# Kernel optimization log

Hardware: AMD Instinct MI355X
Metric: run time of the kernel (lower is better)

Reference implementation:

```python
import math
import jax, jax.numpy as jnp
import numpy as np

D_MODEL = 1024
NUM_HEAD = 16
HEAD_DIM = 64
B = 4
S = 1024


def setup_inputs() -> dict:
    key = jax.random.key(0)
    ks = jax.random.split(key, 11)
    scale = 1.0 / math.sqrt(D_MODEL)
    inp = {
        "x": jax.random.normal(ks[0], (B, S, D_MODEL), dtype=jnp.float32),
        "y": jax.random.normal(ks[1], (B, S, D_MODEL), dtype=jnp.float32),
        "mask": jnp.zeros((S, S), dtype=jnp.float32),
        "Wq": jax.random.uniform(ks[2], (D_MODEL, D_MODEL), jnp.float32, -scale, scale),
        "bq": jax.random.uniform(ks[3], (D_MODEL,), jnp.float32, -scale, scale),
        "Wk": jax.random.uniform(ks[4], (D_MODEL, D_MODEL), jnp.float32, -scale, scale),
        "bk": jax.random.uniform(ks[5], (D_MODEL,), jnp.float32, -scale, scale),
        "Wv": jax.random.uniform(ks[6], (D_MODEL, D_MODEL), jnp.float32, -scale, scale),
        "bv": jax.random.uniform(ks[7], (D_MODEL,), jnp.float32, -scale, scale),
        "Wo": jax.random.uniform(ks[8], (D_MODEL, D_MODEL), jnp.float32, -scale, scale),
        "bo": jax.random.uniform(ks[9], (D_MODEL,), jnp.float32, -scale, scale),
    }
    return inp


def _split_heads(t):
    # (B, S, D) -> (B, H, S, hd)
    b, s, _ = t.shape
    return t.reshape(b, s, NUM_HEAD, HEAD_DIM).transpose(0, 2, 1, 3)


def reference(x, y, mask, Wq, bq, Wk, bk, Wv, bv, Wo, bo):
    q = _split_heads(y @ Wq.T + bq)  # (B, H, S, hd)
    k = _split_heads(x @ Wk.T + bk)
    v = _split_heads(x @ Wv.T + bv)
    scaled = jnp.einsum("bhqd,bhkd->bhqk", q, k) / math.sqrt(HEAD_DIM)
    # torch: scaled.permute(1,0,2,3) + mask  -> (H, B, S, S); second permute is a no-op
    scaled = scaled.transpose(1, 0, 2, 3) + mask
    attention = jax.nn.softmax(scaled, axis=-1)
    attention = jnp.where(jnp.isnan(attention), 0.0, attention)
    # torch sum(dim=1) on (H, B, S, S) sums over BATCH -> (H, S, S)
    attention = jnp.sum(attention, axis=1)
    # broadcast matmul: (H, S, S) @ (B, H, S, hd) -> (B, H, S, hd)
    V = jnp.einsum("hqk,bhkd->bhqd", attention, v)
    V = V.transpose(0, 2, 1, 3).reshape(B, S, NUM_HEAD * HEAD_DIM)
    return V @ Wo.T + bo
```

## Files before the change

### kernel.cpp

```cpp
#include <hip/hip_runtime.h>

typedef unsigned short u16;
typedef unsigned int   u32;
typedef __attribute__((ext_vector_type(8))) short short8;
typedef __attribute__((ext_vector_type(4))) float floatx4;

#define DEV static __device__ __forceinline__

constexpr int S_  = 1024;
constexpr int Dm  = 1024;
constexpr int HD  = 64;


DEV u16 f2b(float f) {
  u32 u = __builtin_bit_cast(u32, f);
  u = u + 0x7fffu + ((u >> 16) & 1u);
  return (u16)(u >> 16);
}
DEV float b2f(u16 h) { u32 u = ((u32)h) << 16; return __builtin_bit_cast(float, u); }

DEV void gld16(const u16* g, u16* l) {
  __builtin_amdgcn_global_load_lds(
      (const __attribute__((address_space(1))) u32*)g,
      (__attribute__((address_space(3))) u32*)l, 16, 0, 0);
}

template<int ROWS, int NT>
DEV void stage_tile(const u16* src, long stride, long kOff, u16* lds, int tid) {
  constexpr int NBLK = ROWS * 8;
  constexpr int NISS = NBLK / NT;
  static_assert(NBLK % NT == 0, "");
  int w = tid >> 6;
  #pragma unroll
  for (int i = 0; i < NISS; ++i) {
    int bi = i * NT + tid;
    int m  = bi >> 3;
    int kb = (bi & 7) ^ (m & 7);
    const u16* g = src + (long)m * stride + kOff + (kb << 3);
    u16* l = lds + ((long)(i * NT + (w << 6)) << 3);
    gld16(g, l);
  }
}

DEV short8 read_frag(const u16* lds, int m, int kb) {
  int off = (m << 6) + ((kb ^ (m & 7)) << 3);
  return *(const short8*)(lds + off);
}

DEV floatx4 mfma16(short8 a, short8 b, floatx4 c) {
  return __builtin_amdgcn_mfma_f32_16x16x32_bf16(a, b, c, 0, 0, 0);
}


struct CvtArgs { const float* s[7]; u16* d[7]; };

__global__ __launch_bounds__(256)
void cvt_all(CvtArgs a) {
  int b = blockIdx.x;
  int t, lb;
  if (b < 4096)      { t = 0; lb = b; }
  else if (b < 8192) { t = 1; lb = b - 4096; }
  else               { t = 2 + ((b - 8192) >> 10); lb = (b - 8192) & 1023; }
  int i = (lb * 256 + (int)threadIdx.x) * 4;
  float4 v = *(const float4*)(a.s[t] + i);
  if (t == 6) {
    v.x = __expf(v.x); v.y = __expf(v.y); v.z = __expf(v.z); v.w = __expf(v.w);
  }
  u32 lo = (u32)f2b(v.x) | ((u32)f2b(v.y) << 16);
  u32 hi = (u32)f2b(v.z) | ((u32)f2b(v.w) << 16);
  uint2 o; o.x = lo; o.y = hi;
  *(uint2*)(a.d[t] + i) = o;
}


struct QkvArgs { const u16* A[3]; const u16* W[3]; const float* bias[3]; u16* C[3]; };

__global__ __launch_bounds__(256, 2)
void gemm_qkv(QkvArgs args) {
  constexpr int CPAD = 136;
  __shared__ u16 smem[128 * CPAD];
  u16* lA = smem;
  u16* lB = smem + 8192;
  int tid = threadIdx.x, lane = tid & 63, w = tid >> 6;
  int wm = w & 1, wn = w >> 1;
  int sel = blockIdx.z;
  bool vt = (sel == 2);
  long mBase = (long)blockIdx.y * 128;
  long nBase = (long)blockIdx.x * 128;
  const u16* Ab = args.A[sel] + mBase * (long)Dm;
  const u16* Bb = args.W[sel] + nBase * (long)Dm;
  const float* bias = args.bias[sel];
  u16* C = args.C[sel];

  floatx4 acc[4][4];
  #pragma unroll
  for (int i = 0; i < 4; ++i)
    #pragma unroll
    for (int j = 0; j < 4; ++j) acc[i][j] = floatx4{0.f, 0.f, 0.f, 0.f};

  for (int kt = 0; kt < Dm; kt += 64) {
    __syncthreads();
    stage_tile<128, 256>(Ab, Dm, kt, lA, tid);
    stage_tile<128, 256>(Bb, Dm, kt, lB, tid);
    __syncthreads();
    #pragma unroll
    for (int ks = 0; ks < 2; ++ks) {
      short8 af[4], bf[4];
      #pragma unroll
      for (int mi = 0; mi < 4; ++mi)
        af[mi] = read_frag(lA, wm*64 + mi*16 + (lane & 15), ks*4 + (lane >> 4));
      #pragma unroll
      for (int ni = 0; ni < 4; ++ni)
        bf[ni] = read_frag(lB, wn*64 + ni*16 + (lane & 15), ks*4 + (lane >> 4));
      #pragma unroll
      for (int mi = 0; mi < 4; ++mi)
        #pragma unroll
        for (int ni = 0; ni < 4; ++ni)
          acc[mi][ni] = mfma16(af[mi], bf[ni], acc[mi][ni]);
    }
  }

  __syncthreads();
  #pragma unroll
  for (int mi = 0; mi < 4; ++mi) {
    int rowb = wm*64 + mi*16 + ((lane >> 4) << 2);
    #pragma unroll
    for (int ni = 0; ni < 4; ++ni) {
      int col = wn*64 + ni*16 + (lane & 15);
      float bv = bias[nBase + col];
      #pragma unroll
      for (int r = 0; r < 4; ++r) {
        float v = acc[mi][ni][r] + bv;
        if (!vt) smem[(rowb + r) * CPAD + col] = f2b(v);
        else     smem[col * CPAD + (rowb + r)] = f2b(v);
      }
    }
  }
  __syncthreads();
  #pragma unroll
  for (int i = 0; i < 8; ++i) {
    int idx = (i * 256 + tid) * 8;
    int r0 = idx >> 7, c0 = idx & 127;
    uint4 v = *(const uint4*)(smem + r0 * CPAD + c0);
    if (!vt) {
      *(uint4*)(C + (mBase + r0) * (long)Dm + nBase + c0) = v;
    } else {
      long m = mBase + c0;
      long ad = ((m >> 10) << 20) + ((nBase + r0) << 10) + (m & 1023);
      *(uint4*)(C + ad) = v;
    }
  }
}


constexpr int MO_BF16 = 0, MO_F32 = 1;

template<int BM, int BN, int WM, int WN, int MODE, bool BIAS, bool ZBH>
__global__ __launch_bounds__(WM*WN*64, 2)
void gemm_bt(const u16* __restrict__ A, const u16* __restrict__ Bmat,
             const float* __restrict__ bias, void* __restrict__ C,
             int K, int ldc) {
  constexpr int NT   = WM * WN * 64;
  constexpr int MI   = BM / WM / 16;
  constexpr int NI   = BN / WN / 16;
  constexpr int WROW = BM / WM;
  constexpr int WCOL = BN / WN;
  constexpr int STG  = (BM + BN) * 64;
  constexpr int CPAD = BN + 8;
  constexpr int CSZ  = BM * CPAD;
  constexpr int SM   = (MODE == MO_F32) ? STG : (STG > CSZ ? STG : CSZ);
  __shared__ u16 smem[SM];
  u16* lA = smem;
  u16* lB = smem + BM * 64;

  int tid = threadIdx.x, lane = tid & 63, w = tid >> 6;
  int wm = w % WM, wn = w / WM;
  long mBase = (long)blockIdx.y * BM;
  long nBase = (long)blockIdx.x * BN;
  long aOff = 0, bOff = 0, cOff = 0;
  if (ZBH) {
    int z = blockIdx.z, bz = z >> 4, h = z & 15;
    aOff = (long)h << 20;
    bOff = (long)z << 16;
    cOff = ((long)bz << 20) + h * HD;
  }
  const u16* Ab = A + aOff + mBase * (long)K;
  const u16* Bb = Bmat + bOff + nBase * (long)K;

  floatx4 acc[MI][NI];
  #pragma unroll
  for (int i = 0; i < MI; ++i)
    #pragma unroll
    for (int j = 0; j < NI; ++j) acc[i][j] = floatx4{0.f, 0.f, 0.f, 0.f};

  for (int kt = 0; kt < K; kt += 64) {
    __syncthreads();
    stage_tile<BM, NT>(Ab, K, kt, lA, tid);
    stage_tile<BN, NT>(Bb, K, kt, lB, tid);
    __syncthreads();
    #pragma unroll
    for (int ks = 0; ks < 2; ++ks) {
      short8 af[MI], bf[NI];
      #pragma unroll
      for (int mi = 0; mi < MI; ++mi)
        af[mi] = read_frag(lA, wm*WROW + mi*16 + (lane & 15), ks*4 + (lane >> 4));
      #pragma unroll
      for (int ni = 0; ni < NI; ++ni)
        bf[ni] = read_frag(lB, wn*WCOL + ni*16 + (lane & 15), ks*4 + (lane >> 4));
      #pragma unroll
      for (int mi = 0; mi < MI; ++mi)
        #pragma unroll
        for (int ni = 0; ni < NI; ++ni)
          acc[mi][ni] = mfma16(af[mi], bf[ni], acc[mi][ni]);
    }
  }

  if (MODE == MO_F32) {
    #pragma unroll
    for (int mi = 0; mi < MI; ++mi) {
      int rowb = wm*WROW + mi*16 + ((lane >> 4) << 2);
      #pragma unroll
      for (int ni = 0; ni < NI; ++ni) {
        int col = wn*WCOL + ni*16 + (lane & 15);
        long n = nBase + col;
        float bv = BIAS ? bias[n] : 0.f;
        #pragma unroll
        for (int r = 0; r < 4; ++r)
          ((float*)C)[cOff + (mBase + rowb + r) * (long)ldc + n] = acc[mi][ni][r] + bv;
      }
    }
  } else {
    __syncthreads();
    #pragma unroll
    for (int mi = 0; mi < MI; ++mi) {
      int rowb = wm*WROW + mi*16 + ((lane >> 4) << 2);
      #pragma unroll
      for (int ni = 0; ni < NI; ++ni) {
        int col = wn*WCOL + ni*16 + (lane & 15);
        float bv = BIAS ? bias[nBase + col] : 0.f;
        #pragma unroll
        for (int r = 0; r < 4; ++r)
          smem[(rowb + r) * CPAD + col] = f2b(acc[mi][ni][r] + bv);
      }
    }
    __syncthreads();
    constexpr int TOT = BM * BN;
    #pragma unroll
    for (int i = 0; i < TOT / (NT * 8); ++i) {
      int idx = (i * NT + tid) * 8;
      int r0 = idx / BN, c0 = idx % BN;
      uint4 v = *(const uint4*)(smem + r0 * CPAD + c0);
      *(uint4*)((u16*)C + cOff + (mBase + r0) * (long)ldc + nBase + c0) = v;
    }
  }
}


__global__ __launch_bounds__(256, 2)
void attn_stats(const u16* __restrict__ Q, const u16* __restrict__ Kw,
                const u16* __restrict__ em, float* __restrict__ lPart) {
  __shared__ u16 lQ[128 * 64];
  __shared__ u16 lK[128 * 64];
  int tid = threadIdx.x, lane = tid & 63, w = tid >> 6;
  int qT = blockIdx.x, h = blockIdx.y, z = blockIdx.z;
  int b = z >> 2, c = z & 3;
  const u16* Qb = Q + ((long)b << 20) + h * HD + (long)qT * 128 * Dm;
  const u16* Kb = Kw + ((long)b << 20) + h * HD + (long)c * 256 * Dm;

  stage_tile<128, 256>(Qb, Dm, 0, lQ, tid);
  __syncthreads();
  short8 af[2][2];
  #pragma unroll
  for (int mi = 0; mi < 2; ++mi)
    #pragma unroll
    for (int ks = 0; ks < 2; ++ks)
      af[mi][ks] = read_frag(lQ, w*32 + mi*16 + (lane & 15), ks*4 + (lane >> 4));

  float lsum[2][4];
  #pragma unroll
  for (int mi = 0; mi < 2; ++mi)
    #pragma unroll
    for (int r = 0; r < 4; ++r) lsum[mi][r] = 0.f;

  for (int kt = 0; kt < 2; ++kt) {
    __syncthreads();
    stage_tile<128, 256>(Kb + (long)kt * 128 * Dm, Dm, 0, lK, tid);
    __syncthreads();
    floatx4 sc[2][8];
    #pragma unroll
    for (int mi = 0; mi < 2; ++mi)
      #pragma unroll
      for (int ni = 0; ni < 8; ++ni) sc[mi][ni] = floatx4{0.f, 0.f, 0.f, 0.f};
    #pragma unroll
    for (int ks = 0; ks < 2; ++ks) {
      short8 bf[8];
      #pragma unroll
      for (int ni = 0; ni < 8; ++ni)
        bf[ni] = read_frag(lK, ni*16 + (lane & 15), ks*4 + (lane >> 4));
      #pragma unroll
      for (int mi = 0; mi < 2; ++mi)
        #pragma unroll
        for (int ni = 0; ni < 8; ++ni)
          sc[mi][ni] = mfma16(af[mi][ks], bf[ni], sc[mi][ni]);
    }
    int q0 = qT*128 + w*32;
    int kBase = c*256 + kt*128;
    #pragma unroll
    for (int mi = 0; mi < 2; ++mi)
      #pragma unroll
      for (int ni = 0; ni < 8; ++ni)
        #pragma unroll
        for (int r = 0; r < 4; ++r) {
          int q  = q0 + mi*16 + ((lane >> 4) << 2) + r;
          int kc = kBase + ni*16 + (lane & 15);
          float e = __expf(sc[mi][ni][r] * 0.125f);
          lsum[mi][r] += e * b2f(em[(long)q * S_ + kc]);
        }
  }
  #pragma unroll
  for (int mi = 0; mi < 2; ++mi)
    #pragma unroll
    for (int r = 0; r < 4; ++r) {
      float l = lsum[mi][r];
      #pragma unroll
      for (int off = 1; off < 16; off <<= 1) l += __shfl_xor(l, off);
      if ((lane & 15) == 0) {
        int q = qT*128 + w*32 + mi*16 + ((lane >> 4) << 2) + r;
        lPart[(long)c * 65536 + ((long)(b * 16 + h) << 10) + q] = l;
      }
    }
}


__global__ __launch_bounds__(256, 2)
void attn_probs(const u16* __restrict__ Q, const u16* __restrict__ Kw,
                const u16* __restrict__ em, const float* __restrict__ lPart,
                u16* __restrict__ att) {
  constexpr int CPAD = 136;
  __shared__ u16 smem[128 * CPAD];
  __shared__ float lL[128];
  u16* lQ = smem;
  u16* lK = smem + 8192;
  int tid = threadIdx.x, lane = tid & 63, w = tid >> 6;
  int wm = w & 1, wn = w >> 1;
  int kT = blockIdx.x, qT = blockIdx.y, h = blockIdx.z;
  long q0 = (long)qT * 128, k0 = (long)kT * 128;

  floatx4 pa[4][4];
  #pragma unroll
  for (int i = 0; i < 4; ++i)
    #pragma unroll
    for (int j = 0; j < 4; ++j) pa[i][j] = floatx4{0.f, 0.f, 0.f, 0.f};

  for (int b = 0; b < 4; ++b) {
    __syncthreads();
    stage_tile<128, 256>(Q + ((long)b << 20) + h * HD + q0 * Dm, Dm, 0, lQ, tid);
    stage_tile<128, 256>(Kw + ((long)b << 20) + h * HD + k0 * Dm, Dm, 0, lK, tid);
    if (tid < 128) {
      long base = ((long)(b * 16 + h) << 10) + q0 + tid;
      float l = 0.f;
      #pragma unroll
      for (int cch = 0; cch < 4; ++cch) l += lPart[(long)cch * 65536 + base];
      lL[tid] = (l > 0.f) ? 1.f / l : 0.f;
    }
    __syncthreads();
    floatx4 sc[4][4];
    #pragma unroll
    for (int i = 0; i < 4; ++i)
      #pragma unroll
      for (int j = 0; j < 4; ++j) sc[i][j] = floatx4{0.f, 0.f, 0.f, 0.f};
    #pragma unroll
    for (int ks = 0; ks < 2; ++ks) {
      short8 af[4], bf[4];
      #pragma unroll
      for (int mi = 0; mi < 4; ++mi)
        af[mi] = read_frag(lQ, wm*64 + mi*16 + (lane & 15), ks*4 + (lane >> 4));
      #pragma unroll
      for (int ni = 0; ni < 4; ++ni)
        bf[ni] = read_frag(lK, wn*64 + ni*16 + (lane & 15), ks*4 + (lane >> 4));
      #pragma unroll
      for (int mi = 0; mi < 4; ++mi)
        #pragma unroll
        for (int ni = 0; ni < 4; ++ni)
          sc[mi][ni] = mfma16(af[mi], bf[ni], sc[mi][ni]);
    }
    #pragma unroll
    for (int mi = 0; mi < 4; ++mi)
      #pragma unroll
      for (int r = 0; r < 4; ++r) {
        int qq = wm*64 + mi*16 + ((lane >> 4) << 2) + r;
        float li = lL[qq];
        #pragma unroll
        for (int ni = 0; ni < 4; ++ni)
          pa[mi][ni][r] += __expf(sc[mi][ni][r] * 0.125f) * li;
      }
  }

  __syncthreads();
  #pragma unroll
  for (int mi = 0; mi < 4; ++mi)
    #pragma unroll
    for (int ni = 0; ni < 4; ++ni) {
      int kc = wn*64 + ni*16 + (lane & 15);
      #pragma unroll
      for (int r = 0; r < 4; ++r) {
        int qq = wm*64 + mi*16 + ((lane >> 4) << 2) + r;
        float mk = b2f(em[(q0 + qq) * S_ + k0 + kc]);
        smem[qq * CPAD + kc] = f2b(pa[mi][ni][r] * mk);
      }
    }
  __syncthreads();
  #pragma unroll
  for (int i = 0; i < 8; ++i) {
    int idx = (i * 256 + tid) * 8;
    int r0 = idx >> 7, c0 = idx & 127;
    uint4 v = *(const uint4*)(smem + r0 * CPAD + c0);
    *(uint4*)(att + ((long)h << 20) + (q0 + r0) * S_ + k0 + c0) = v;
  }
}


extern "C" void kernel_launch(void* const* d_in, const int* in_sizes, int n_in,
                              void* d_out, int out_size, void* d_ws, size_t ws_size,
                              hipStream_t stream) {
  const float* x    = (const float*)d_in[0];
  const float* y    = (const float*)d_in[1];
  const float* mask = (const float*)d_in[2];
  const float* Wq   = (const float*)d_in[3];
  const float* bq   = (const float*)d_in[4];
  const float* Wk   = (const float*)d_in[5];
  const float* bk   = (const float*)d_in[6];
  const float* Wv   = (const float*)d_in[7];
  const float* bv   = (const float*)d_in[8];
  const float* Wo   = (const float*)d_in[9];
  const float* bo   = (const float*)d_in[10];

  char* ws = (char*)d_ws;
  const long MB = 1024 * 1024;
  u16*  Qw   = (u16*)(ws + 0);
  u16*  Kw   = (u16*)(ws + 8 * MB);
  u16*  Vt   = (u16*)(ws + 16 * MB);
  u16*  attv = (u16*)(ws + 24 * MB);
  float* lPart = (float*)(ws + 24 * MB);
  u16*  em   = (u16*)(ws + 25 * MB);
  u16*  Wob  = (u16*)(ws + 33 * MB);
  u16*  att  = (u16*)(ws + 35 * MB);
  u16*  yb   = (u16*)(ws + 35 * MB);
  u16*  xb   = (u16*)(ws + 43 * MB);
  u16*  Wqb  = (u16*)(ws + 51 * MB);
  u16*  Wkb  = (u16*)(ws + 53 * MB);
  u16*  Wvb  = (u16*)(ws + 55 * MB);

  dim3 blk(256);
  CvtArgs ca;
  ca.s[0] = y;  ca.s[1] = x;  ca.s[2] = Wq;  ca.s[3] = Wk;  ca.s[4] = Wv;  ca.s[5] = Wo;  ca.s[6] = mask;
  ca.d[0] = yb; ca.d[1] = xb; ca.d[2] = Wqb; ca.d[3] = Wkb; ca.d[4] = Wvb; ca.d[5] = Wob; ca.d[6] = em;
  cvt_all<<<dim3(13312), blk, 0, stream>>>(ca);

  QkvArgs qa;
  qa.A[0] = yb;  qa.A[1] = xb;  qa.A[2] = xb;
  qa.W[0] = Wqb; qa.W[1] = Wkb; qa.W[2] = Wvb;
  qa.bias[0] = bq; qa.bias[1] = bk; qa.bias[2] = bv;
  qa.C[0] = Qw;  qa.C[1] = Kw;  qa.C[2] = Vt;
  gemm_qkv<<<dim3(8, 32, 3), blk, 0, stream>>>(qa);

  attn_stats<<<dim3(8, 16, 16), blk, 0, stream>>>(Qw, Kw, em, lPart);
  attn_probs<<<dim3(8, 8, 16), blk, 0, stream>>>(Qw, Kw, em, lPart, att);

  gemm_bt<128,64,2,2,MO_BF16,false,true><<<dim3(1, 8, 64), blk, 0, stream>>>(att, Vt, nullptr, attv, 1024, 1024);
  gemm_bt<64,128,2,2,MO_F32,true,false><<<dim3(8, 64), blk, 0, stream>>>(attv, Wob, bo, d_out, 1024, 1024);
}
```

Baseline: 240.2 us.

## Fold softmax scale into Q, add permuted exp-mask layout for stats loads

Moves the 1/sqrt(hd) scale into the Q projection epilogue so the attention kernels skip a multiply per score. Adds a separate kernel that writes the exp-mask both in the original layout and in a permuted layout, so each lane in attn_stats loads its 8 mask values with one 16-byte load instead of 8 scattered scalar loads. In attn_probs the mask multiply moves to the coalesced store loop, which adds an extra bf16 rounding of the probabilities before masking. It also adds a small launch and 2MB of workspace for the second mask copy.

```diff
diff --git a/kernel.cpp b/kernel.cpp
--- a/kernel.cpp
+++ b/kernel.cpp
@@ -52,7 +52,7 @@
 }
 
 
-struct CvtArgs { const float* s[7]; u16* d[7]; };
+struct CvtArgs { const float* s[6]; u16* d[6]; };
 
 __global__ __launch_bounds__(256)
 void cvt_all(CvtArgs a) {
@@ -63,13 +63,44 @@
   else               { t = 2 + ((b - 8192) >> 10); lb = (b - 8192) & 1023; }
   int i = (lb * 256 + (int)threadIdx.x) * 4;
   float4 v = *(const float4*)(a.s[t] + i);
-  if (t == 6) {
-    v.x = __expf(v.x); v.y = __expf(v.y); v.z = __expf(v.z); v.w = __expf(v.w);
-  }
   u32 lo = (u32)f2b(v.x) | ((u32)f2b(v.y) << 16);
   u32 hi = (u32)f2b(v.z) | ((u32)f2b(v.w) << 16);
   uint2 o; o.x = lo; o.y = hi;
   *(uint2*)(a.d[t] + i) = o;
+}
+
+
+__global__ __launch_bounds__(256)
+void emask_prep(const float* __restrict__ mask, u16* __restrict__ em,
+                u16* __restrict__ emr) {
+  __shared__ u16 lp[8 * 1024];
+  int tid = threadIdx.x;
+  long q0 = (long)blockIdx.x * 8;
+  #pragma unroll
+  for (int rr = 0; rr < 8; ++rr) {
+    long q = q0 + rr;
+    float4 v = *(const float4*)(mask + q * 1024 + tid * 4);
+    u16 e0 = f2b(__expf(v.x)), e1 = f2b(__expf(v.y));
+    u16 e2 = f2b(__expf(v.z)), e3 = f2b(__expf(v.w));
+    u32 lo = (u32)e0 | ((u32)e1 << 16);
+    u32 hi = (u32)e2 | ((u32)e3 << 16);
+    uint2 o; o.x = lo; o.y = hi;
+    *(uint2*)(em + q * 1024 + tid * 4) = o;
+    int k = tid * 4;
+    u16 es[4] = {e0, e1, e2, e3};
+    #pragma unroll
+    for (int j = 0; j < 4; ++j) {
+      int kk = k + j;
+      lp[rr * 1024 + ((kk & 15) << 6) + (kk >> 4)] = es[j];
+    }
+  }
+  __syncthreads();
+  #pragma unroll
+  for (int jj = 0; jj < 4; ++jj) {
+    int o = jj * 2048 + tid * 8;
+    uint4 v = *(const uint4*)(lp + o);
+    *(uint4*)(emr + q0 * 1024 + o) = v;
+  }
 }
 
 
@@ -85,6 +116,7 @@
   int wm = w & 1, wn = w >> 1;
   int sel = blockIdx.z;
   bool vt = (sel == 2);
+  float scl = (sel == 0) ? 0.125f : 1.0f;
   long mBase = (long)blockIdx.y * 128;
   long nBase = (long)blockIdx.x * 128;
   const u16* Ab = args.A[sel] + mBase * (long)Dm;
@@ -130,7 +162,7 @@
       float bv = bias[nBase + col];
       #pragma unroll
       for (int r = 0; r < 4; ++r) {
-        float v = acc[mi][ni][r] + bv;
+        float v = (acc[mi][ni][r] + bv) * scl;
         if (!vt) smem[(rowb + r) * CPAD + col] = f2b(v);
         else     smem[col * CPAD + (rowb + r)] = f2b(v);
       }
@@ -258,7 +290,7 @@
 
 __global__ __launch_bounds__(256, 2)
 void attn_stats(const u16* __restrict__ Q, const u16* __restrict__ Kw,
-                const u16* __restrict__ em, float* __restrict__ lPart) {
+                const u16* __restrict__ emr, float* __restrict__ lPart) {
   __shared__ u16 lQ[128 * 64];
   __shared__ u16 lK[128 * 64];
   int tid = threadIdx.x, lane = tid & 63, w = tid >> 6;
@@ -303,19 +335,21 @@
         for (int ni = 0; ni < 8; ++ni)
           sc[mi][ni] = mfma16(af[mi][ks], bf[ni], sc[mi][ni]);
     }
-    int q0 = qT*128 + w*32;
-    int kBase = c*256 + kt*128;
+    int q0w = qT*128 + w*32;
+    int iBase = (c*256 + kt*128) >> 4;
     #pragma unroll
     for (int mi = 0; mi < 2; ++mi)
       #pragma unroll
-      for (int ni = 0; ni < 8; ++ni)
-        #pragma unroll
-        for (int r = 0; r < 4; ++r) {
-          int q  = q0 + mi*16 + ((lane >> 4) << 2) + r;
-          int kc = kBase + ni*16 + (lane & 15);
-          float e = __expf(sc[mi][ni][r] * 0.125f);
-          lsum[mi][r] += e * b2f(em[(long)q * S_ + kc]);
-        }
+      for (int r = 0; r < 4; ++r) {
+        int q = q0w + mi*16 + ((lane >> 4) << 2) + r;
+        uint4 ev = *(const uint4*)(emr + ((long)q << 10) + ((lane & 15) << 6) + iBase);
+        const u16* e8 = (const u16*)&ev;
+        float a = 0.f;
+        #pragma unroll
+        for (int ni = 0; ni < 8; ++ni)
+          a += __expf(sc[mi][ni][r]) * b2f(e8[ni]);
+        lsum[mi][r] += a;
+      }
   }
   #pragma unroll
   for (int mi = 0; mi < 2; ++mi)
@@ -392,7 +426,7 @@
         float li = lL[qq];
         #pragma unroll
         for (int ni = 0; ni < 4; ++ni)
-          pa[mi][ni][r] += __expf(sc[mi][ni][r] * 0.125f) * li;
+          pa[mi][ni][r] += __expf(sc[mi][ni][r]) * li;
       }
   }
 
@@ -405,8 +439,7 @@
       #pragma unroll
       for (int r = 0; r < 4; ++r) {
         int qq = wm*64 + mi*16 + ((lane >> 4) << 2) + r;
-        float mk = b2f(em[(q0 + qq) * S_ + k0 + kc]);
-        smem[qq * CPAD + kc] = f2b(pa[mi][ni][r] * mk);
+        smem[qq * CPAD + kc] = f2b(pa[mi][ni][r]);
       }
     }
   __syncthreads();
@@ -414,8 +447,14 @@
   for (int i = 0; i < 8; ++i) {
     int idx = (i * 256 + tid) * 8;
     int r0 = idx >> 7, c0 = idx & 127;
-    uint4 v = *(const uint4*)(smem + r0 * CPAD + c0);
-    *(uint4*)(att + ((long)h << 20) + (q0 + r0) * S_ + k0 + c0) = v;
+    uint4 v  = *(const uint4*)(smem + r0 * CPAD + c0);
+    uint4 ev = *(const uint4*)(em + (q0 + r0) * S_ + k0 + c0);
+    const u16* pv = (const u16*)&v;
+    const u16* ee = (const u16*)&ev;
+    u16 ov[8];
+    #pragma unroll
+    for (int j = 0; j < 8; ++j) ov[j] = f2b(b2f(pv[j]) * b2f(ee[j]));
+    *(uint4*)(att + ((long)h << 20) + (q0 + r0) * S_ + k0 + c0) = *(uint4*)ov;
   }
 }
 
@@ -443,6 +482,7 @@
   u16*  attv = (u16*)(ws + 24 * MB);
   float* lPart = (float*)(ws + 24 * MB);
   u16*  em   = (u16*)(ws + 25 * MB);
+  u16*  emr  = (u16*)(ws + 27 * MB);
   u16*  Wob  = (u16*)(ws + 33 * MB);
   u16*  att  = (u16*)(ws + 35 * MB);
   u16*  yb   = (u16*)(ws + 35 * MB);
@@ -453,9 +493,10 @@
 
   dim3 blk(256);
   CvtArgs ca;
-  ca.s[0] = y;  ca.s[1] = x;  ca.s[2] = Wq;  ca.s[3] = Wk;  ca.s[4] = Wv;  ca.s[5] = Wo;  ca.s[6] = mask;
-  ca.d[0] = yb; ca.d[1] = xb; ca.d[2] = Wqb; ca.d[3] = Wkb; ca.d[4] = Wvb; ca.d[5] = Wob; ca.d[6] = em;
-  cvt_all<<<dim3(13312), blk, 0, stream>>>(ca);
+  ca.s[0] = y;  ca.s[1] = x;  ca.s[2] = Wq;  ca.s[3] = Wk;  ca.s[4] = Wv;  ca.s[5] = Wo;
+  ca.d[0] = yb; ca.d[1] = xb; ca.d[2] = Wqb; ca.d[3] = Wkb; ca.d[4] = Wvb; ca.d[5] = Wob;
+  cvt_all<<<dim3(12288), blk, 0, stream>>>(ca);
+  emask_prep<<<dim3(128), blk, 0, stream>>>(mask, em, emr);
 
   QkvArgs qa;
   qa.A[0] = yb;  qa.A[1] = xb;  qa.A[2] = xb;
@@ -464,7 +505,7 @@
   qa.C[0] = Qw;  qa.C[1] = Kw;  qa.C[2] = Vt;
   gemm_qkv<<<dim3(8, 32, 3), blk, 0, stream>>>(qa);
 
-  attn_stats<<<dim3(8, 16, 16), blk, 0, stream>>>(Qw, Kw, em, lPart);
+  attn_stats<<<dim3(8, 16, 16), blk, 0, stream>>>(Qw, Kw, emr, lPart);
   attn_probs<<<dim3(8, 8, 16), blk, 0, stream>>>(Qw, Kw, em, lPart, att);
 
   gemm_bt<128,64,2,2,MO_BF16,false,true><<<dim3(1, 8, 64), blk, 0, stream>>>(att, Vt, nullptr, attv, 1024, 1024);
```

New measurement: 250.8 us. 1.04x slower.
